# Performance work log

Hardware: AMD Instinct MI355X
Metric: run time of the kernel (lower is better)

Reference implementation:

```python
import jax, jax.numpy as jnp
import numpy as np

B, C, H, W = 4, 128, 128, 128
E, K, HID = 11, 6, 512  # num_experts, active_experts, 4*dim


def setup_inputs() -> dict:
    key = jax.random.key(0)
    ks = jax.random.split(key, 5)
    return {
        "x": jax.random.normal(ks[0], (B, C, H, W), jnp.float32),
        "gate_w": jax.random.normal(ks[1], (E, C), jnp.float32) * 0.02,
        "gate_b": jnp.zeros((E,), jnp.float32),
        "w1": jax.random.normal(ks[2], (E, HID, C), jnp.float32) * 0.02,
        "b1": jnp.zeros((E, HID), jnp.float32),
        "w2": jax.random.normal(ks[3], (E, C, HID), jnp.float32) * 0.02,
        "b2": jnp.zeros((E, C), jnp.float32),
    }


def reference(x, gate_w, gate_b, w1, b1, w2, b2):
    n_experts = gate_w.shape[0]
    k = K  # active_experts
    # channels-last for per-pixel routing / 1x1-conv-as-matmul
    xcl = jnp.transpose(x, (0, 2, 3, 1))  # [B,H,W,C]
    # --- router (1x1 conv gate + softmax over experts + top-k) ---
    logits = jnp.einsum('bhwc,ec->bhwe', xcl, gate_w) + gate_b
    scores = jax.nn.softmax(logits, axis=-1)            # [B,H,W,E]
    topk_p, topk_i = jax.lax.top_k(scores, k)           # [B,H,W,K]
    topk_p = topk_p / topk_p.sum(axis=-1, keepdims=True)
    # scatter routing weights into dense per-expert mask (indices distinct)
    onehot = jax.nn.one_hot(topk_i, n_experts, dtype=x.dtype)  # [B,H,W,K,E]
    mask = jnp.einsum('bhwke,bhwk->bhwe', onehot, topk_p)      # [B,H,W,E]
    # --- dense expert compute, masked accumulate (as in original loop) ---
    acc = jnp.zeros_like(xcl)
    for e in range(n_experts):
        h = jax.nn.gelu(jnp.einsum('bhwc,dc->bhwd', xcl, w1[e]) + b1[e],
                        approximate=False)  # torch GELU is exact erf form
        oe = jnp.einsum('bhwd,cd->bhwc', h, w2[e]) + b2[e]
        acc = acc + mask[..., e:e + 1] * oe
    y = x + jnp.transpose(acc, (0, 3, 1, 2))  # back to NCHW
    # --- load-balancing aux loss ---
    mean_prob = scores.mean(axis=(0, 1, 2))            # [E]
    mean_load = onehot.sum(axis=3).mean(axis=(0, 1, 2))  # binary mask mean, [E]
    aux_loss = n_experts * jnp.sum(mean_prob * mean_load)
    return (y, aux_loss)
```

## Files before the change

kernel.cpp:

```cpp
#include <hip/hip_runtime.h>
#include <stdint.h>

#define C_   128
#define HW_  16384
#define CHW_ (C_*HW_)
#define N_   65536
#define E_   11
#define K_   6
#define HID_ 512

typedef __attribute__((ext_vector_type(8))) _Float16 half8;
typedef __attribute__((ext_vector_type(2))) _Float16 h2;
typedef __attribute__((ext_vector_type(2))) __fp16 fp16v2;
typedef __attribute__((ext_vector_type(16))) float float16v;
typedef __attribute__((ext_vector_type(2))) unsigned uint2v;

#define GLD(g, s) __builtin_amdgcn_global_load_lds( \
    (const __attribute__((address_space(1))) unsigned int*)(uintptr_t)(g), \
    (__attribute__((address_space(3))) unsigned int*)(unsigned int)(uintptr_t)(s), 16, 0, 0)

__device__ __forceinline__ h2 pkrtz(float a, float b){
  union { fp16v2 f; h2 h; } u;
  u.f = __builtin_amdgcn_cvt_pkrtz(a, b);
  return u.h;
}
__device__ __forceinline__ h2 gelu2h(h2 v, h2 wr2){
  h2 u = v * v;
  h2 s = u * (h2)(_Float16)(-0.00076957f) + (h2)(_Float16)(0.0147811f);
  s = s * u + (h2)(_Float16)(-0.126434f);
  s = s * u + (h2)(_Float16)(0.795742f);
  h2 p = v * s;
  h2 phi = p * (h2)(_Float16)(0.5f) + (h2)(_Float16)(0.5f);
  return v * wr2 * phi;
}
__device__ __forceinline__ void pswap32(unsigned &a, unsigned &b){
#if __has_builtin(__builtin_amdgcn_permlane32_swap)
  uint2v r = __builtin_amdgcn_permlane32_swap(a, b, false, false);
  a = r.x; b = r.y;
#else
  asm volatile("v_permlane32_swap_b32 %0, %1" : "+v"(a), "+v"(b));
#endif
}

__global__ __launch_bounds__(256) void k_convert(const float* __restrict__ w1,
                                                 const float* __restrict__ w2,
                                                 const float* __restrict__ b1,
                                                 unsigned short* __restrict__ wimg,
                                                 unsigned short* __restrict__ b1h,
                                                 float* __restrict__ auxsum){
  int t = blockIdx.x * 256 + threadIdx.x;
  if (t < 23) auxsum[t] = 0.0f;
  if (t >= 185856) return;
  if (t >= 180224){
    int t2 = t - 180224;
    int rec = t2 >> 5, j5 = t2 & 31;
    int hi = j5 >> 4, j = j5 & 15;
    int e = rec >> 4, hc = rec & 15;
    int row = (j & 3) + 8 * (j >> 2) + 4 * hi;
    union { _Float16 h; unsigned short u; } cv;
    cv.h = (_Float16)b1[e * 512 + hc * 32 + row];
    b1h[rec * 32 + j5] = cv.u;
    return;
  }
  const float* src;
  size_t dst;
  if (t < 90112){
    int e = t >> 13, hid = (t >> 4) & 511, c8 = t & 15;
    src = w1 + (size_t)t * 8;
    int rec = e * 16 + (hid >> 5);
    int kc = c8 >> 1, half = c8 & 1;
    int l = (hid & 31) | (half << 5);
    dst = (size_t)rec * 8192 + kc * 512 + l * 8;
  } else {
    int u = t - 90112;
    int e = u >> 13, cc = (u >> 6) & 127, hd8 = u & 63;
    src = w2 + (size_t)u * 8;
    int rec = e * 16 + (hd8 >> 2);
    int kc2 = (hd8 >> 1) & 1, half = hd8 & 1, ct = cc >> 5;
    int l = (cc & 31) | (half << 5);
    dst = (size_t)rec * 8192 + 4096 + (ct * 2 + kc2) * 512 + l * 8;
  }
  float4 a = *(const float4*)src, b = *(const float4*)(src + 4);
  union { _Float16 h[8]; uint4 v; } u4;
  u4.h[0] = (_Float16)a.x; u4.h[1] = (_Float16)a.y;
  u4.h[2] = (_Float16)a.z; u4.h[3] = (_Float16)a.w;
  u4.h[4] = (_Float16)b.x; u4.h[5] = (_Float16)b.y;
  u4.h[6] = (_Float16)b.z; u4.h[7] = (_Float16)b.w;
  *(uint4*)(wimg + dst) = u4.v;
}

__global__ __launch_bounds__(256) void k_pre(const float* __restrict__ x,
                                             const float* __restrict__ gw,
                                             const float* __restrict__ gb,
                                             const float* __restrict__ b2,
                                             unsigned short* __restrict__ xcl,
                                             float* __restrict__ mask,
                                             float* __restrict__ auxsum){
  __shared__ __align__(16) float tt[64 * 130];
  __shared__ __align__(16) float g[E_ * C_];
  __shared__ float gbs[E_];
  __shared__ float ap[E_], al[E_];
  int tid = threadIdx.x;
  int pix0 = blockIdx.x * 64;
  int b = pix0 >> 14, hw0 = pix0 & 16383;
  const float* xb = x + (size_t)b * CHW_ + hw0;

  for (int i = tid; i < E_ * C_; i += 256) g[i] = gw[i];
  if (tid < E_) { gbs[tid] = gb[tid]; ap[tid] = 0.f; al[tid] = 0.f; }

  #pragma unroll 4
  for (int it = 0; it < 32; ++it){
    int flat = it * 256 + tid;
    int c = flat >> 6, p = flat & 63;
    tt[p * 130 + c] = xb[c * HW_ + p];
  }
  __syncthreads();
  #pragma unroll 4
  for (int it = 0; it < 16; ++it){
    int u = it * 256 + tid;
    int p = u >> 6, cc = u & 63;
    float f0 = tt[p * 130 + 2 * cc], f1 = tt[p * 130 + 2 * cc + 1];
    union { h2 h; unsigned u; } pv;
    pv.h = pkrtz(f0, f1);
    ((unsigned*)xcl)[(size_t)(pix0 + p) * 64 + cc] = pv.u;
  }

  int p = tid >> 2, t4 = tid & 3;
  float lg[E_];
  #pragma unroll
  for (int e = 0; e < E_; ++e) lg[e] = (t4 == 0) ? gbs[e] : 0.f;
  const float2* ttrow = (const float2*)(tt + p * 130 + t4 * 32);
  #pragma unroll 4
  for (int j2 = 0; j2 < 16; ++j2){
    float2 xv = ttrow[j2];
    #pragma unroll
    for (int e = 0; e < E_; ++e){
      float2 gv = *(const float2*)(g + e * C_ + t4 * 32 + j2 * 2);
      lg[e] = fmaf(xv.x, gv.x, lg[e]);
      lg[e] = fmaf(xv.y, gv.y, lg[e]);
    }
  }
  #pragma unroll
  for (int e = 0; e < E_; ++e){
    lg[e] += __shfl_xor(lg[e], 1, 64);
    lg[e] += __shfl_xor(lg[e], 2, 64);
  }
  float mx = lg[0];
  #pragma unroll
  for (int e = 1; e < E_; ++e) mx = fmaxf(mx, lg[e]);
  float pr[E_]; float s = 0.f;
  #pragma unroll
  for (int e = 0; e < E_; ++e){ pr[e] = expf(lg[e] - mx); s += pr[e]; }
  float inv = 1.0f / s;
  #pragma unroll
  for (int e = 0; e < E_; ++e) pr[e] *= inv;

  unsigned selmask = 0; float wsum = 0.f;
  for (int k = 0; k < K_; ++k){
    float bv = -1.f; int bi = 0;
    #pragma unroll
    for (int e = 0; e < E_; ++e){
      bool better = (((selmask >> e) & 1u) == 0u) && (pr[e] > bv);
      bv = better ? pr[e] : bv;
      bi = better ? e : bi;
    }
    selmask |= 1u << bi; wsum += bv;
  }
  float invw = 1.0f / wsum;
  if (t4 == 0){
    int pix = pix0 + p;
    #pragma unroll
    for (int e = 0; e < E_; ++e){
      bool sel = (selmask >> e) & 1u;
      mask[(size_t)pix * E_ + e] = sel ? pr[e] * invw : 0.f;
      atomicAdd(&ap[e], pr[e]);
      if (sel) atomicAdd(&al[e], 1.0f);
    }
  }
  __syncthreads();
  if (tid < E_){
    atomicAdd(&auxsum[tid], ap[tid]);
    atomicAdd(&auxsum[E_ + tid], al[tid]);
  }
  if (blockIdx.x == 0 && tid < 64){
    int nz = 0;
    for (int idx = tid; idx < E_ * C_; idx += 64)
      nz |= (__float_as_uint(b2[idx]) != 0u) ? 1 : 0;
    if (nz) atomicOr((int*)(auxsum + 22), 1);
  }
}

__global__ __launch_bounds__(256, 1) void k_ffn(const unsigned short* __restrict__ xcl,
                                                const unsigned short* __restrict__ wimg,
                                                const unsigned short* __restrict__ b1h,
                                                const float* __restrict__ b2,
                                                const float* __restrict__ mask,
                                                const float* __restrict__ aux,
                                                const float* __restrict__ x,
                                                float* __restrict__ y){
  __shared__ unsigned char smem[65536];
  int tid = threadIdx.x;
  int w = tid >> 6, l = tid & 63;
  int l31 = l & 31, hi = l >> 5;
  int hi4 = hi * 4;
  int pix0 = blockIdx.x * 256;
  int off = (blockIdx.x % 11) * 16;
  const unsigned char* wimgB = (const unsigned char*)wimg;
  const unsigned char* b1hB  = (const unsigned char*)b1h;

  if (blockIdx.x == 0 && tid == 0){
    float s = 0.f;
    const float invN = 1.0f / (float)N_;
    for (int e = 0; e < E_; ++e)
      s += (aux[e] * invN) * (aux[E_ + e] * invN);
    y[(size_t)N_ * C_] = (float)E_ * s;
  }

  half8 Xf0[8], Xf1[8];
  {
    const unsigned short* xr0 = xcl + ((size_t)(pix0 + w * 64 + l31) << 7) + hi * 8;
    #pragma unroll
    for (int kc = 0; kc < 8; ++kc){
      Xf0[kc] = *(const half8*)(xr0 + kc * 16);
      Xf1[kc] = *(const half8*)(xr0 + 4096 + kc * 16);
    }
  }

  uint4 bhA[4], bhB[4];
  const size_t mrowA = (size_t)(pix0 + w * 64 + l31) * 11;
  const size_t mrowB = mrowA + 32 * 11;

  #pragma unroll
  for (int k = 0; k < 2; ++k){
    int rec = off + k;
    const unsigned char* gs = wimgB + (size_t)rec * 16384 + w * 4096 + l * 16;
    unsigned char* dst = smem + k * 16384 + w * 4096;
    GLD(gs, dst);            GLD(gs + 1024, dst + 1024);
    GLD(gs + 2048, dst + 2048); GLD(gs + 3072, dst + 3072);
    const unsigned char* bp = b1hB + rec * 64 + hi * 32;
    bhA[2 * k]     = *(const uint4*)(bp);
    bhA[2 * k + 1] = *(const uint4*)(bp + 16);
  }
  float wrnA = mask[mrowA + (off >> 4)];
  float wrnB = mask[mrowB + (off >> 4)];
  __syncthreads();

  float16v facc0[4], facc1[4];
  #pragma unroll
  for (int ct = 0; ct < 4; ++ct){ facc0[ct] = (float16v)0.0f; facc1[ct] = (float16v)0.0f; }
  h2 wr2A = (h2)(_Float16)0.0f, wr2B = (h2)(_Float16)0.0f;

#define G1(WB, H0, H1)                                                              \
  {                                                                                 \
    half8 a_[8];                                                                    \
    _Pragma("unroll")                                                               \
    for (int kc_ = 0; kc_ < 8; ++kc_)                                               \
      a_[kc_] = *(const half8*)((WB) + kc_ * 1024 + l * 16);                        \
    _Pragma("unroll")                                                               \
    for (int kc_ = 0; kc_ < 8; ++kc_){                                              \
      H0 = __builtin_amdgcn_mfma_f32_32x32x16_f16(a_[kc_], Xf0[kc_], H0, 0, 0, 0);  \
      H1 = __builtin_amdgcn_mfma_f32_32x32x16_f16(a_[kc_], Xf1[kc_], H1, 0, 0, 0);  \
    }                                                                               \
  }

#define EPI(HACC, BH0, BH1, WR2, CV0, CV1)                                          \
  {                                                                                 \
    union { uint4 v[2]; h2 h[8]; } bu_;                                             \
    bu_.v[0] = BH0; bu_.v[1] = BH1;                                                 \
    unsigned pd_[8];                                                                \
    _Pragma("unroll")                                                               \
    for (int k_ = 0; k_ < 8; ++k_){                                                 \
      h2 v_ = pkrtz(HACC[2 * k_], HACC[2 * k_ + 1]);                                \
      v_ = v_ + bu_.h[k_];                                                          \
      union { h2 h; unsigned u; } g_;                                               \
      g_.h = gelu2h(v_, WR2);                                                       \
      pd_[k_] = g_.u;                                                               \
    }                                                                               \
    pswap32(pd_[0], pd_[2]); pswap32(pd_[1], pd_[3]);                               \
    pswap32(pd_[4], pd_[6]); pswap32(pd_[5], pd_[7]);                               \
    union { unsigned u[4]; half8 s; } c0_, c1_;                                     \
    c0_.u[0] = pd_[0]; c0_.u[1] = pd_[1]; c0_.u[2] = pd_[2]; c0_.u[3] = pd_[3];     \
    c1_.u[0] = pd_[4]; c1_.u[1] = pd_[5]; c1_.u[2] = pd_[6]; c1_.u[3] = pd_[7];     \
    CV0 = c0_.s; CV1 = c1_.s;                                                       \
  }

#define G2(WB, A00, A01, A10, A11)                                                  \
  {                                                                                 \
    _Pragma("unroll")                                                               \
    for (int ct_ = 0; ct_ < 4; ++ct_){                                              \
      half8 w0_ = *(const half8*)((WB) + 8192 + (ct_ * 2 + 0) * 1024 + l * 16);     \
      half8 w1_ = *(const half8*)((WB) + 8192 + (ct_ * 2 + 1) * 1024 + l * 16);     \
      facc0[ct_] = __builtin_amdgcn_mfma_f32_32x32x16_f16(w0_, A00, facc0[ct_], 0, 0, 0); \
      facc0[ct_] = __builtin_amdgcn_mfma_f32_32x32x16_f16(w1_, A01, facc0[ct_], 0, 0, 0); \
      facc1[ct_] = __builtin_amdgcn_mfma_f32_32x32x16_f16(w0_, A10, facc1[ct_], 0, 0, 0); \
      facc1[ct_] = __builtin_amdgcn_mfma_f32_32x32x16_f16(w1_, A11, facc1[ct_], 0, 0, 0); \
    }                                                                               \
  }

#define SUPER_BODY(J, BHC, BHL)                                                     \
  {                                                                                 \
    asm volatile("s_waitcnt vmcnt(4)" ::: "memory");                                \
    __builtin_amdgcn_s_barrier();                                                   \
    __builtin_amdgcn_sched_barrier(0);                                              \
         \
                                             \
    {                                                                               \
      unsigned char* dbuf_ = smem + ((((J) + 1) & 1) << 15);                        \
      _Pragma("unroll")                                                             \
      for (int k_ = 0; k_ < 2; ++k_){                                               \
        int rn_ = 2 * (J) + 2 + k_ + off; if (rn_ >= 176) rn_ -= 176;               \
        const unsigned char* gs_ = wimgB + (size_t)rn_ * 16384 + w * 4096 + l * 16; \
        unsigned char* dst_ = dbuf_ + k_ * 16384 + w * 4096;                        \
        GLD(gs_, dst_);             GLD(gs_ + 1024, dst_ + 1024);                   \
        GLD(gs_ + 2048, dst_ + 2048); GLD(gs_ + 3072, dst_ + 3072);                 \
      }                                                                             \
      __builtin_amdgcn_sched_barrier(0);                                            \
      _Pragma("unroll")                                                             \
      for (int k_ = 0; k_ < 2; ++k_){                                               \
        int rn_ = 2 * (J) + 2 + k_ + off; if (rn_ >= 176) rn_ -= 176;               \
        const unsigned char* bp_ = b1hB + rn_ * 64 + hi * 32;                       \
        BHL[2 * k_]     = *(const uint4*)(bp_);                                     \
        BHL[2 * k_ + 1] = *(const uint4*)(bp_ + 16);                                \
      }                                                                             \
    }                                                                               \
    __builtin_amdgcn_sched_barrier(0);                                              \
    if (((J) & 7) == 0){           \
      _Float16 wa_ = (_Float16)wrnA, wb_ = (_Float16)wrnB;                          \
      wr2A = (h2){wa_, wa_}; wr2B = (h2){wb_, wb_};                                 \
      int rn_ = 2 * (J) + 16 + off; if (rn_ >= 176) rn_ -= 176;                     \
      wrnA = mask[mrowA + (rn_ >> 4)];                                              \
      wrnB = mask[mrowB + (rn_ >> 4)];                                              \
    }                                                                               \
    const unsigned char* wb_ = smem + (((J) & 1) << 15);                            \
    float16v hA0 = (float16v)0.0f, hA1 = (float16v)0.0f;                            \
    float16v hB0 = (float16v)0.0f, hB1 = (float16v)0.0f;                            \
    G1(wb_, hA0, hA1);                                                              \
    G1(wb_ + 16384, hB0, hB1);                     \
    half8 cA00, cA01, cA10, cA11;                                                   \
    EPI(hA0, BHC[0], BHC[1], wr2A, cA00, cA01);                                     \
    EPI(hA1, BHC[0], BHC[1], wr2B, cA10, cA11);                                     \
    G2(wb_, cA00, cA01, cA10, cA11);               \
    half8 cB00, cB01, cB10, cB11;                                                   \
    EPI(hB0, BHC[2], BHC[3], wr2A, cB00, cB01);                                     \
    EPI(hB1, BHC[2], BHC[3], wr2B, cB10, cB11);                                     \
    G2(wb_ + 16384, cB00, cB01, cB10, cB11);                                        \
  }

  #pragma unroll 1
  for (int jj = 0; jj < 44; ++jj){
    SUPER_BODY(2 * jj,     bhA, bhB);
    SUPER_BODY(2 * jj + 1, bhB, bhA);
  }
#undef SUPER_BODY
#undef G2
#undef EPI
#undef G1

  __syncthreads();
  float* lds_t = (float*)smem;
  float* b2t   = (float*)(smem + 17408);
  for (int idx = tid; idx < 1536; idx += 256){
    int cc = idx / 12, ee = idx - cc * 12;
    b2t[idx] = (ee < 11) ? b2[ee * 128 + cc] : 0.f;
  }
  int b2nz = ((const int*)aux)[22];

#define DUMPF(F)                                                                     \
  _Pragma("unroll")                                                                  \
  for (int ct_ = 0; ct_ < 4; ++ct_)                                                  \
    _Pragma("unroll")                                                                \
    for (int rg_ = 0; rg_ < 16; ++rg_)                                               \
      lds_t[(ct_ * 32 + (rg_ & 3) + 8 * (rg_ >> 2) + hi4) * 33 + l31] = F[ct_][rg_];

  #pragma unroll 1
  for (int r = 0; r < 8; ++r){
    __syncthreads();
    if (w == (r >> 1)){
      if (r & 1) { DUMPF(facc1) } else { DUMPF(facc0) }
    }
    __syncthreads();
    int c = tid >> 1, ph = (tid & 1) << 4;
    int pixg = pix0 + r * 32 + ph;
    size_t base = (size_t)(pixg >> 14) * CHW_ + (size_t)c * HW_ + (pixg & 16383);
    float av[16];
    #pragma unroll
    for (int k = 0; k < 16; ++k) av[k] = lds_t[c * 33 + ph + k];
    if (b2nz){
      #pragma unroll
      for (int k = 0; k < 16; ++k){
        const float* mr = mask + (size_t)(pixg + k) * 11;
        #pragma unroll
        for (int e = 0; e < 11; ++e) av[k] = fmaf(mr[e], b2t[c * 12 + e], av[k]);
      }
    }
    #pragma unroll
    for (int q = 0; q < 4; ++q){
      float4 xv = *(const float4*)(x + base + q * 4);
      float4 o = {av[4 * q] + xv.x, av[4 * q + 1] + xv.y,
                  av[4 * q + 2] + xv.z, av[4 * q + 3] + xv.w};
      *(float4*)(y + base + q * 4) = o;
    }
  }
#undef DUMPF
}

extern "C" void kernel_launch(void* const* d_in, const int* in_sizes, int n_in,
                              void* d_out, int out_size, void* d_ws, size_t ws_size,
                              hipStream_t stream){
  const float* x  = (const float*)d_in[0];
  const float* gw = (const float*)d_in[1];
  const float* gb = (const float*)d_in[2];
  const float* w1 = (const float*)d_in[3];
  const float* b1 = (const float*)d_in[4];
  const float* w2 = (const float*)d_in[5];
  const float* b2 = (const float*)d_in[6];
  float* y = (float*)d_out;
  char* ws = (char*)d_ws;

  unsigned short* xcl  = (unsigned short*)ws;
  unsigned short* wimg = (unsigned short*)(ws + 16777216);
  float* mask   = (float*)(ws + 19660800);
  float* auxsum = (float*)(ws + 22544384);
  unsigned short* b1h  = (unsigned short*)(ws + 22544480);

  hipLaunchKernelGGL(k_convert, dim3(726),  dim3(256), 0, stream, w1, w2, b1, wimg, b1h, auxsum);
  hipLaunchKernelGGL(k_pre,     dim3(1024), dim3(256), 0, stream, x, gw, gb, b2, xcl, mask, auxsum);
  hipLaunchKernelGGL(k_ffn,     dim3(256),  dim3(256), 0, stream, xcl, wimg, b1h, b2, mask, auxsum, x, y);
}
```

Measured before the change: 355.0 us.

## Split expert hidden-chunk loop across two wave groups with LDS reduction

Doubles the FFN block to 512 threads and splits the 176 weight records between two groups of four waves, starting half a ring apart. Each iteration now stages and processes one record per group instead of two records per wave, which gives each CU more waves to hide latency. The two groups' fp32 partial accumulators are summed through LDS before the residual write. The trade-off is that launch_bounds(512,2) tightens the register budget while large MFMA accumulators stay live, which risks spills, and the per-iteration wait is now vmcnt(0) instead of vmcnt(4).

New measurement: 398.5 us. +12.3%, slower.

```diff
diff --git a/kernel.cpp b/kernel.cpp
--- a/kernel.cpp
+++ b/kernel.cpp
@@ -190,7 +190,7 @@
   }
 }
 
-__global__ __launch_bounds__(256, 1) void k_ffn(const unsigned short* __restrict__ xcl,
+__global__ __launch_bounds__(512, 2) void k_ffn(const unsigned short* __restrict__ xcl,
                                                 const unsigned short* __restrict__ wimg,
                                                 const unsigned short* __restrict__ b1h,
                                                 const float* __restrict__ b2,
@@ -203,6 +203,7 @@
   int w = tid >> 6, l = tid & 63;
   int l31 = l & 31, hi = l >> 5;
   int hi4 = hi * 4;
+  int t = w >> 2, wq = w & 3;
   int pix0 = blockIdx.x * 256;
   int off = (blockIdx.x % 11) * 16;
   const unsigned char* wimgB = (const unsigned char*)wimg;
@@ -218,7 +219,7 @@
 
   half8 Xf0[8], Xf1[8];
   {
-    const unsigned short* xr0 = xcl + ((size_t)(pix0 + w * 64 + l31) << 7) + hi * 8;
+    const unsigned short* xr0 = xcl + ((size_t)(pix0 + wq * 64 + l31) << 7) + hi * 8;
     #pragma unroll
     for (int kc = 0; kc < 8; ++kc){
       Xf0[kc] = *(const half8*)(xr0 + kc * 16);
@@ -226,29 +227,35 @@
     }
   }
 
-  uint4 bhA[4], bhB[4];
-  const size_t mrowA = (size_t)(pix0 + w * 64 + l31) * 11;
+  const size_t mrowA = (size_t)(pix0 + wq * 64 + l31) * 11;
   const size_t mrowB = mrowA + 32 * 11;
 
-  #pragma unroll
-  for (int k = 0; k < 2; ++k){
-    int rec = off + k;
-    const unsigned char* gs = wimgB + (size_t)rec * 16384 + w * 4096 + l * 16;
-    unsigned char* dst = smem + k * 16384 + w * 4096;
-    GLD(gs, dst);            GLD(gs + 1024, dst + 1024);
-    GLD(gs + 2048, dst + 2048); GLD(gs + 3072, dst + 3072);
-    const unsigned char* bp = b1hB + rec * 64 + hi * 32;
-    bhA[2 * k]     = *(const uint4*)(bp);
-    bhA[2 * k + 1] = *(const uint4*)(bp + 16);
-  }
-  float wrnA = mask[mrowA + (off >> 4)];
-  float wrnB = mask[mrowB + (off >> 4)];
-  __syncthreads();
+  int rb = off + 88 * t; if (rb >= 176) rb -= 176;
+
+  uint4 bhA[2], bhB[2];
+  {
+    int r10 = off + 88; if (r10 >= 176) r10 -= 176;
+    const unsigned char* g0 = wimgB + (size_t)off * 16384 + w * 2048 + l * 16;
+    GLD(g0, smem + w * 2048);             GLD(g0 + 1024, smem + w * 2048 + 1024);
+    const unsigned char* g1 = wimgB + (size_t)r10 * 16384 + w * 2048 + l * 16;
+    GLD(g1, smem + 16384 + w * 2048);     GLD(g1 + 1024, smem + 16384 + w * 2048 + 1024);
+    const unsigned char* bp = b1hB + rb * 64 + hi * 32;
+    bhA[0] = *(const uint4*)(bp);
+    bhA[1] = *(const uint4*)(bp + 16);
+  }
+  h2 wr2A, wr2B;
+  float wrnA, wrnB;
+  {
+    int e0 = rb >> 4;
+    _Float16 wa = (_Float16)mask[mrowA + e0], wb = (_Float16)mask[mrowB + e0];
+    wr2A = (h2){wa, wa}; wr2B = (h2){wb, wb};
+    int en = e0 + 1; if (en == 11) en = 0;
+    wrnA = mask[mrowA + en]; wrnB = mask[mrowB + en];
+  }
 
   float16v facc0[4], facc1[4];
   #pragma unroll
   for (int ct = 0; ct < 4; ++ct){ facc0[ct] = (float16v)0.0f; facc1[ct] = (float16v)0.0f; }
-  h2 wr2A = (h2)(_Float16)0.0f, wr2B = (h2)(_Float16)0.0f;
 
 #define G1(WB, H0, H1)                                                              \
   {                                                                                 \
@@ -297,61 +304,51 @@
     }                                                                               \
   }
 
-#define SUPER_BODY(J, BHC, BHL)                                                     \
+#define BODY(J, BHC, BHL)                                                           \
   {                                                                                 \
-    asm volatile("s_waitcnt vmcnt(4)" ::: "memory");                                \
+    asm volatile("s_waitcnt vmcnt(0)" ::: "memory");                                \
     __builtin_amdgcn_s_barrier();                                                   \
     __builtin_amdgcn_sched_barrier(0);                                              \
-         \
-                                             \
+    int sr0_ = off + (J) + 1; if (sr0_ >= 176) sr0_ -= 176;                         \
+    int sr1_ = sr0_ + 88;     if (sr1_ >= 176) sr1_ -= 176;                         \
+    unsigned char* dbuf_ = smem + ((((J) + 1) & 1) << 15);                          \
     {                                                                               \
-      unsigned char* dbuf_ = smem + ((((J) + 1) & 1) << 15);                        \
-      _Pragma("unroll")                                                             \
-      for (int k_ = 0; k_ < 2; ++k_){                                               \
-        int rn_ = 2 * (J) + 2 + k_ + off; if (rn_ >= 176) rn_ -= 176;               \
-        const unsigned char* gs_ = wimgB + (size_t)rn_ * 16384 + w * 4096 + l * 16; \
-        unsigned char* dst_ = dbuf_ + k_ * 16384 + w * 4096;                        \
-        GLD(gs_, dst_);             GLD(gs_ + 1024, dst_ + 1024);                   \
-        GLD(gs_ + 2048, dst_ + 2048); GLD(gs_ + 3072, dst_ + 3072);                 \
-      }                                                                             \
-      __builtin_amdgcn_sched_barrier(0);                                            \
-      _Pragma("unroll")                                                             \
-      for (int k_ = 0; k_ < 2; ++k_){                                               \
-        int rn_ = 2 * (J) + 2 + k_ + off; if (rn_ >= 176) rn_ -= 176;               \
-        const unsigned char* bp_ = b1hB + rn_ * 64 + hi * 32;                       \
-        BHL[2 * k_]     = *(const uint4*)(bp_);                                     \
-        BHL[2 * k_ + 1] = *(const uint4*)(bp_ + 16);                                \
-      }                                                                             \
+      const unsigned char* g0_ = wimgB + (size_t)sr0_ * 16384 + w * 2048 + l * 16;  \
+      GLD(g0_, dbuf_ + w * 2048);                                                   \
+      GLD(g0_ + 1024, dbuf_ + w * 2048 + 1024);                                     \
+      const unsigned char* g1_ = wimgB + (size_t)sr1_ * 16384 + w * 2048 + l * 16;  \
+      GLD(g1_, dbuf_ + 16384 + w * 2048);                                           \
+      GLD(g1_ + 1024, dbuf_ + 16384 + w * 2048 + 1024);                             \
     }                                                                               \
     __builtin_amdgcn_sched_barrier(0);                                              \
-    if (((J) & 7) == 0){           \
+    {                                                                               \
+      int srm_ = t ? sr1_ : sr0_;                                                   \
+      const unsigned char* bp_ = b1hB + srm_ * 64 + hi * 32;                        \
+      BHL[0] = *(const uint4*)(bp_);                                                \
+      BHL[1] = *(const uint4*)(bp_ + 16);                                           \
+    }                                                                               \
+    int rc_ = rb + (J); if (rc_ >= 176) rc_ -= 176;                                 \
+    if ((rc_ & 15) == 0 && (J) != 0){             \
       _Float16 wa_ = (_Float16)wrnA, wb_ = (_Float16)wrnB;                          \
       wr2A = (h2){wa_, wa_}; wr2B = (h2){wb_, wb_};                                 \
-      int rn_ = 2 * (J) + 16 + off; if (rn_ >= 176) rn_ -= 176;                     \
-      wrnA = mask[mrowA + (rn_ >> 4)];                                              \
-      wrnB = mask[mrowB + (rn_ >> 4)];                                              \
-    }                                                                               \
-    const unsigned char* wb_ = smem + (((J) & 1) << 15);                            \
-    float16v hA0 = (float16v)0.0f, hA1 = (float16v)0.0f;                            \
-    float16v hB0 = (float16v)0.0f, hB1 = (float16v)0.0f;                            \
-    G1(wb_, hA0, hA1);                                                              \
-    G1(wb_ + 16384, hB0, hB1);                     \
-    half8 cA00, cA01, cA10, cA11;                                                   \
-    EPI(hA0, BHC[0], BHC[1], wr2A, cA00, cA01);                                     \
-    EPI(hA1, BHC[0], BHC[1], wr2B, cA10, cA11);                                     \
-    G2(wb_, cA00, cA01, cA10, cA11);               \
-    half8 cB00, cB01, cB10, cB11;                                                   \
-    EPI(hB0, BHC[2], BHC[3], wr2A, cB00, cB01);                                     \
-    EPI(hB1, BHC[2], BHC[3], wr2B, cB10, cB11);                                     \
-    G2(wb_ + 16384, cB00, cB01, cB10, cB11);                                        \
+      int en_ = (rc_ >> 4) + 1; if (en_ == 11) en_ = 0;                             \
+      wrnA = mask[mrowA + en_]; wrnB = mask[mrowB + en_];                           \
+    }                                                                               \
+    const unsigned char* cb_ = smem + (((J) & 1) << 15) + t * 16384;                \
+    float16v h0_ = (float16v)0.0f, h1_ = (float16v)0.0f;                            \
+    G1(cb_, h0_, h1_);                                                              \
+    half8 c00_, c01_, c10_, c11_;                                                   \
+    EPI(h0_, BHC[0], BHC[1], wr2A, c00_, c01_);                                     \
+    EPI(h1_, BHC[0], BHC[1], wr2B, c10_, c11_);                                     \
+    G2(cb_, c00_, c01_, c10_, c11_);                                                \
   }
 
   #pragma unroll 1
   for (int jj = 0; jj < 44; ++jj){
-    SUPER_BODY(2 * jj,     bhA, bhB);
-    SUPER_BODY(2 * jj + 1, bhB, bhA);
-  }
-#undef SUPER_BODY
+    BODY(2 * jj,     bhA, bhB);
+    BODY(2 * jj + 1, bhB, bhA);
+  }
+#undef BODY
 #undef G2
 #undef EPI
 #undef G1
@@ -359,7 +356,7 @@
   __syncthreads();
   float* lds_t = (float*)smem;
   float* b2t   = (float*)(smem + 17408);
-  for (int idx = tid; idx < 1536; idx += 256){
+  for (int idx = tid; idx < 1536; idx += 512){
     int cc = idx / 12, ee = idx - cc * 12;
     b2t[idx] = (ee < 11) ? b2[ee * 128 + cc] : 0.f;
   }
@@ -371,6 +368,12 @@
     _Pragma("unroll")                                                                \
     for (int rg_ = 0; rg_ < 16; ++rg_)                                               \
       lds_t[(ct_ * 32 + (rg_ & 3) + 8 * (rg_ >> 2) + hi4) * 33 + l31] = F[ct_][rg_];
+#define ADDF(F)                                                                      \
+  _Pragma("unroll")                                                                  \
+  for (int ct_ = 0; ct_ < 4; ++ct_)                                                  \
+    _Pragma("unroll")                                                                \
+    for (int rg_ = 0; rg_ < 16; ++rg_)                                               \
+      lds_t[(ct_ * 32 + (rg_ & 3) + 8 * (rg_ >> 2) + hi4) * 33 + l31] += F[ct_][rg_];
 
   #pragma unroll 1
   for (int r = 0; r < 8; ++r){
@@ -379,29 +382,33 @@
       if (r & 1) { DUMPF(facc1) } else { DUMPF(facc0) }
     }
     __syncthreads();
-    int c = tid >> 1, ph = (tid & 1) << 4;
-    int pixg = pix0 + r * 32 + ph;
+    if (w == 4 + (r >> 1)){
+      if (r & 1) { ADDF(facc1) } else { ADDF(facc0) }
+    }
+    __syncthreads();
+    int c = tid >> 2, p8 = (tid & 3) << 3;
+    int pixg = pix0 + r * 32 + p8;
     size_t base = (size_t)(pixg >> 14) * CHW_ + (size_t)c * HW_ + (pixg & 16383);
-    float av[16];
+    float av[8];
     #pragma unroll
-    for (int k = 0; k < 16; ++k) av[k] = lds_t[c * 33 + ph + k];
+    for (int k = 0; k < 8; ++k) av[k] = lds_t[c * 33 + p8 + k];
     if (b2nz){
       #pragma unroll
-      for (int k = 0; k < 16; ++k){
+      for (int k = 0; k < 8; ++k){
         const float* mr = mask + (size_t)(pixg + k) * 11;
         #pragma unroll
         for (int e = 0; e < 11; ++e) av[k] = fmaf(mr[e], b2t[c * 12 + e], av[k]);
       }
     }
-    #pragma unroll
-    for (int q = 0; q < 4; ++q){
-      float4 xv = *(const float4*)(x + base + q * 4);
-      float4 o = {av[4 * q] + xv.x, av[4 * q + 1] + xv.y,
-                  av[4 * q + 2] + xv.z, av[4 * q + 3] + xv.w};
-      *(float4*)(y + base + q * 4) = o;
-    }
+    float4 xv0 = *(const float4*)(x + base);
+    float4 xv1 = *(const float4*)(x + base + 4);
+    float4 o0 = {av[0] + xv0.x, av[1] + xv0.y, av[2] + xv0.z, av[3] + xv0.w};
+    float4 o1 = {av[4] + xv1.x, av[5] + xv1.y, av[6] + xv1.z, av[7] + xv1.w};
+    *(float4*)(y + base) = o0;
+    *(float4*)(y + base + 4) = o1;
   }
 #undef DUMPF
+#undef ADDF
 }
 
 extern "C" void kernel_launch(void* const* d_in, const int* in_sizes, int n_in,
@@ -425,5 +432,5 @@
 
   hipLaunchKernelGGL(k_convert, dim3(726),  dim3(256), 0, stream, w1, w2, b1, wimg, b1h, auxsum);
   hipLaunchKernelGGL(k_pre,     dim3(1024), dim3(256), 0, stream, x, gw, gb, b2, xcl, mask, auxsum);
-  hipLaunchKernelGGL(k_ffn,     dim3(256),  dim3(256), 0, stream, xcl, wimg, b1h, b2, mask, auxsum, x, y);
-}
+  hipLaunchKernelGGL(k_ffn,     dim3(256),  dim3(512), 0, stream, xcl, wimg, b1h, b2, mask, auxsum, x, y);
+}
```
